# Performance work log

Measured on AMD Instinct MI355X. Metric: run time of the kernel, lower is better.

Reference implementation:

```python
import jax, jax.numpy as jnp
import numpy as np

N = 500_000          # minibatch nodes
NUM_NODES = 1_000_000  # embedding table rows
F0 = 500_000         # raw feature table rows for ntype 0
DIN = 256            # raw feature dim for ntype 0
D = 128              # embed_size


def setup_inputs() -> dict:
    key = jax.random.key(0)
    k0, k1, k2, k3, k4, k5 = jax.random.split(key, 6)
    feat0 = jax.random.normal(k0, (F0, DIN), dtype=jnp.float32)
    # xavier-uniform-ish scale for the projection
    lim = float(np.sqrt(6.0 / (DIN + D)))
    W0 = jax.random.uniform(k1, (DIN, D), dtype=jnp.float32, minval=-lim, maxval=lim)
    # node_embeds initialized uniform(-1, 1)
    emb_table = jax.random.uniform(k2, (NUM_NODES, D), dtype=jnp.float32, minval=-1.0, maxval=1.0)
    node_ids = jax.random.randint(k3, (N,), 0, NUM_NODES, dtype=jnp.int32)
    node_tids = jax.random.randint(k4, (N,), 0, 2, dtype=jnp.int32)
    type_ids = jax.random.randint(k5, (N,), 0, F0, dtype=jnp.int32)
    return {"feat0": feat0, "W0": W0, "emb_table": emb_table,
            "node_ids": node_ids, "node_tids": node_tids, "type_ids": type_ids}


def reference(feat0, W0, emb_table, node_ids, node_tids, type_ids):
    # Original loops over node types, building per-type blocks and an index
    # map idx so that the final embeds[idx] restores the original node order.
    # That is equivalent to, per node i:
    #   out[i] = feat0[type_ids[i]] @ W0   if node_tids[i] == 0 (featured type)
    #   out[i] = emb_table[node_ids[i]]    if node_tids[i] == 1 (featureless)
    proj = feat0[type_ids] @ W0          # [N, D] gather + tall-skinny matmul
    emb = emb_table[node_ids]            # [N, D] embedding lookup
    is_featured = (node_tids == 0)[:, None]
    return jnp.where(is_featured, proj, emb)
```

## Files before the change

### kernel.cpp

```cpp
#include <hip/hip_runtime.h>
#include <hip/hip_bf16.h>

#define DIN 256
#define DOUT 128
#define NB 64

using short8  = __attribute__((ext_vector_type(8))) short;
using floatx4 = __attribute__((ext_vector_type(4))) float;

__device__ __forceinline__ unsigned short f2bf(float f) {
    union { float f; unsigned u; } x; x.f = f;
    unsigned u = x.u;
    unsigned r = u + 0x7fffu + ((u >> 16) & 1u);
    return (unsigned short)(r >> 16);
}

__global__ void w0_pack_kernel(const float* __restrict__ W0,
                               unsigned short* __restrict__ Bfrag) {
    int e = blockIdx.x * blockDim.x + threadIdx.x;
    int j  = e & 7;
    int l  = (e >> 3) & 63;
    int ks = (e >> 9) & 7;
    int wt = e >> 12;
    int k = ks * 32 + (l >> 4) * 8 + j;
    int c = wt * 16 + (l & 15);
    Bfrag[e] = f2bf(W0[k * DOUT + c]);
}

__global__ __launch_bounds__(512) void fused_embed_kernel(
    const float* __restrict__ feat0,
    const float* __restrict__ emb_table,
    const unsigned short* __restrict__ Bfrag,
    const int* __restrict__ node_ids,
    const int* __restrict__ node_tids,
    const int* __restrict__ type_ids,
    float* __restrict__ out,
    int n)
{
    __shared__ unsigned short sA[NB * DIN];
    __shared__ unsigned char  sFeat[NB];

    const int t    = threadIdx.x;
    const int base = blockIdx.x * NB;
    const int w    = t >> 6;
    const int l    = t & 63;

    short8 bf[8];
    {
        const short8* bsrc = reinterpret_cast<const short8*>(Bfrag);
        #pragma unroll
        for (int ks = 0; ks < 8; ++ks)
            bf[ks] = bsrc[(w * 8 + ks) * 64 + l];
    }

    {
        const int m = t >> 3;
        const int p = t & 7;
        const int i = base + m;
        int tid = 1;
        if (i < n) tid = node_tids[i];
        const bool featured = (i < n) && (tid == 0);
        if (p == 0) sFeat[m] = featured ? 1 : 0;

        if (featured) {
            const float* src = feat0 + (long long)type_ids[i] * DIN;
            float4 v[8];
            #pragma unroll
            for (int j = 0; j < 8; ++j)
                v[j] = *reinterpret_cast<const float4*>(src + j * 32 + p * 4);
            #pragma unroll
            for (int j = 0; j < 8; ++j) {
                const int k = j * 32 + p * 4;
                ushort4 pk;
                pk.x = f2bf(v[j].x); pk.y = f2bf(v[j].y);
                pk.z = f2bf(v[j].z); pk.w = f2bf(v[j].w);
                const unsigned addr =
                    (unsigned)(m * 512 + k * 2) ^ ((unsigned)(m & 7) << 4);
                *reinterpret_cast<ushort4*>(reinterpret_cast<char*>(sA) + addr) = pk;
            }
        } else if (i < n) {
            const float4* src = reinterpret_cast<const float4*>(
                emb_table + (long long)node_ids[i] * DOUT);
            float4* dst = reinterpret_cast<float4*>(out + (long long)i * DOUT);
            float4 v[4];
            #pragma unroll
            for (int j = 0; j < 4; ++j) v[j] = src[p + j * 8];
            #pragma unroll
            for (int j = 0; j < 4; ++j) dst[p + j * 8] = v[j];
        }
    }
    __syncthreads();

    const int lr = l & 15;
    const int kg = l >> 4;

    floatx4 acc[4];
    #pragma unroll
    for (int rt = 0; rt < 4; ++rt) acc[rt] = (floatx4){0.f, 0.f, 0.f, 0.f};

    #pragma unroll
    for (int ks = 0; ks < 8; ++ks) {
        #pragma unroll
        for (int rt = 0; rt < 4; ++rt) {
            const int row = rt * 16 + lr;
            const unsigned aaddr =
                (unsigned)(row * 512 + ks * 64 + kg * 16) ^ ((unsigned)(row & 7) << 4);
            const short8 af = *reinterpret_cast<const short8*>(
                reinterpret_cast<const char*>(sA) + aaddr);
            acc[rt] = __builtin_amdgcn_mfma_f32_16x16x32_bf16(af, bf[ks], acc[rt], 0, 0, 0);
        }
    }

    const int col = w * 16 + lr;
    #pragma unroll
    for (int rt = 0; rt < 4; ++rt) {
        #pragma unroll
        for (int r = 0; r < 4; ++r) {
            const int row = rt * 16 + kg * 4 + r;
            if (sFeat[row])
                out[(long long)(base + row) * DOUT + col] = acc[rt][r];
        }
    }
}

extern "C" void kernel_launch(void* const* d_in, const int* in_sizes, int n_in,
                              void* d_out, int out_size, void* d_ws, size_t ws_size,
                              hipStream_t stream) {
    const float* feat0      = (const float*)d_in[0];
    const float* W0         = (const float*)d_in[1];
    const float* emb_table  = (const float*)d_in[2];
    const int*   node_ids   = (const int*)d_in[3];
    const int*   node_tids  = (const int*)d_in[4];
    const int*   type_ids   = (const int*)d_in[5];
    float*       out        = (float*)d_out;
    const int n = in_sizes[3];

    unsigned short* Bfrag = (unsigned short*)d_ws;

    hipLaunchKernelGGL(w0_pack_kernel, dim3((DIN * DOUT) / 256), dim3(256),
                       0, stream, W0, Bfrag);

    const int grid = (n + NB - 1) / NB;
    hipLaunchKernelGGL(fused_embed_kernel, dim3(grid), dim3(512), 0, stream,
                       feat0, emb_table, Bfrag, node_ids, node_tids, type_ids, out, n);
}
```

Before: 158.9 us.

## Persistent blocks with double-buffered LDS to overlap gathers with MFMA compute

New measurement: 206.5 us. 1.3x slower.

```diff
diff --git a/kernel.cpp b/kernel.cpp
--- a/kernel.cpp
+++ b/kernel.cpp
@@ -27,7 +27,7 @@
     Bfrag[e] = f2bf(W0[k * DOUT + c]);
 }
 
-__global__ __launch_bounds__(512) void fused_embed_kernel(
+__global__ __launch_bounds__(512, 4) void fused_embed_kernel(
     const float* __restrict__ feat0,
     const float* __restrict__ emb_table,
     const unsigned short* __restrict__ Bfrag,
@@ -35,15 +35,22 @@
     const int* __restrict__ node_tids,
     const int* __restrict__ type_ids,
     float* __restrict__ out,
-    int n)
+    int n, int ntiles, int tpb)
 {
-    __shared__ unsigned short sA[NB * DIN];
-    __shared__ unsigned char  sFeat[NB];
+    __shared__ unsigned short sA[2][NB * DIN];
+    __shared__ unsigned char  sFeat[2][NB];
 
-    const int t    = threadIdx.x;
-    const int base = blockIdx.x * NB;
-    const int w    = t >> 6;
-    const int l    = t & 63;
+    const int t  = threadIdx.x;
+    const int w  = t >> 6;
+    const int l  = t & 63;
+    const int m  = t >> 3;
+    const int p  = t & 7;
+    const int lr = l & 15;
+    const int kg = l >> 4;
+
+    const int t0 = blockIdx.x * tpb;
+    const int t1 = (t0 + tpb < ntiles) ? (t0 + tpb) : ntiles;
+    if (t0 >= t1) return;
 
     short8 bf[8];
     {
@@ -53,21 +60,31 @@
             bf[ks] = bsrc[(w * 8 + ks) * 64 + l];
     }
 
-    {
-        const int m = t >> 3;
-        const int p = t & 7;
-        const int i = base + m;
-        int tid = 1;
-        if (i < n) tid = node_tids[i];
-        const bool featured = (i < n) && (tid == 0);
-        if (p == 0) sFeat[m] = featured ? 1 : 0;
+    int tidA = -1, gtA = 0, gnA = 0;
+    int tidB = -1, gtB = 0, gnB = 0;
+    float4 v[8];
 
-        if (featured) {
-            const float* src = feat0 + (long long)type_ids[i] * DIN;
-            float4 v[8];
+    auto loadIdx = [&](int tt, int& tid, int& gt, int& gn) {
+        const int i = tt * NB + m;
+        if (i < n) { tid = node_tids[i]; gt = type_ids[i]; gn = node_ids[i]; }
+        else tid = -1;
+    };
+    auto issueGather = [&](int tid, int gt, int gn) {
+        if (tid == 0) {
+            const float* src = feat0 + (long long)gt * DIN;
             #pragma unroll
             for (int j = 0; j < 8; ++j)
                 v[j] = *reinterpret_cast<const float4*>(src + j * 32 + p * 4);
+        } else if (tid == 1) {
+            const float4* src = reinterpret_cast<const float4*>(
+                emb_table + (long long)gn * DOUT);
+            #pragma unroll
+            for (int j = 0; j < 4; ++j) v[j] = src[p + j * 8];
+        }
+    };
+    auto commit = [&](int buf, int tt, int tid) {
+        if (tid == 0) {
+            char* basep = reinterpret_cast<char*>(&sA[buf][0]);
             #pragma unroll
             for (int j = 0; j < 8; ++j) {
                 const int k = j * 32 + p * 4;
@@ -76,50 +93,81 @@
                 pk.z = f2bf(v[j].z); pk.w = f2bf(v[j].w);
                 const unsigned addr =
                     (unsigned)(m * 512 + k * 2) ^ ((unsigned)(m & 7) << 4);
-                *reinterpret_cast<ushort4*>(reinterpret_cast<char*>(sA) + addr) = pk;
+                *reinterpret_cast<ushort4*>(basep + addr) = pk;
             }
-        } else if (i < n) {
-            const float4* src = reinterpret_cast<const float4*>(
-                emb_table + (long long)node_ids[i] * DOUT);
+        } else if (tid == 1) {
+            const int i = tt * NB + m;
             float4* dst = reinterpret_cast<float4*>(out + (long long)i * DOUT);
-            float4 v[4];
-            #pragma unroll
-            for (int j = 0; j < 4; ++j) v[j] = src[p + j * 8];
             #pragma unroll
             for (int j = 0; j < 4; ++j) dst[p + j * 8] = v[j];
         }
-    }
+    };
+
+    loadIdx(t0, tidA, gtA, gnA);
+    if (t0 + 1 < t1) loadIdx(t0 + 1, tidB, gtB, gnB);
+    issueGather(tidA, gtA, gnA);
+    if (p == 0) sFeat[0][m] = (tidA == 0) ? 1 : 0;
+    commit(0, t0, tidA);
+    tidA = tidB; gtA = gtB; gnA = gnB;
     __syncthreads();
 
-    const int lr = l & 15;
-    const int kg = l >> 4;
+    for (int tt = t0; tt < t1; ++tt) {
+        const int cur = (tt - t0) & 1;
+        const int nxt = cur ^ 1;
+        const bool hasNext = (tt + 1 < t1);
 
-    floatx4 acc[4];
-    #pragma unroll
-    for (int rt = 0; rt < 4; ++rt) acc[rt] = (floatx4){0.f, 0.f, 0.f, 0.f};
+        if (hasNext) {
+            issueGather(tidA, gtA, gnA);
+            if (p == 0) sFeat[nxt][m] = (tidA == 0) ? 1 : 0;
+        }
+        if (tt + 2 < t1) loadIdx(tt + 2, tidB, gtB, gnB); else tidB = -1;
 
-    #pragma unroll
-    for (int ks = 0; ks < 8; ++ks) {
+        floatx4 acc[4];
+        #pragma unroll
+        for (int rt = 0; rt < 4; ++rt) acc[rt] = (floatx4){0.f, 0.f, 0.f, 0.f};
+        const char* basep = reinterpret_cast<const char*>(&sA[cur][0]);
+        #pragma unroll
+        for (int ks = 0; ks < 8; ++ks) {
+            #pragma unroll
+            for (int rt = 0; rt < 4; ++rt) {
+                const int row = rt * 16 + lr;
+                const unsigned aaddr =
+                    (unsigned)(row * 512 + ks * 64 + kg * 16) ^ ((unsigned)(row & 7) << 4);
+                const short8 af = *reinterpret_cast<const short8*>(basep + aaddr);
+                acc[rt] = __builtin_amdgcn_mfma_f32_16x16x32_bf16(af, bf[ks], acc[rt], 0, 0, 0);
+            }
+        }
+
+        if (hasNext) commit(nxt, tt + 1, tidA);
+
+        bool ok[4];
+        #pragma unroll
+        for (int r = 0; r < 4; ++r) ok[r] = sFeat[cur][kg * 4 + r] != 0
+                                            || false;
+        #pragma unroll
+        for (int r = 0; r < 4; ++r) ok[r] = false;
+        unsigned char okb[16];
+        #pragma unroll
+        for (int rt = 0; rt < 4; ++rt)
+            #pragma unroll
+            for (int r = 0; r < 4; ++r)
+                okb[rt * 4 + r] = sFeat[cur][rt * 16 + kg * 4 + r];
+
+        __syncthreads();
+
+        const int col  = w * 16 + lr;
+        const int base = tt * NB;
         #pragma unroll
         for (int rt = 0; rt < 4; ++rt) {
-            const int row = rt * 16 + lr;
-            const unsigned aaddr =
-                (unsigned)(row * 512 + ks * 64 + kg * 16) ^ ((unsigned)(row & 7) << 4);
-            const short8 af = *reinterpret_cast<const short8*>(
-                reinterpret_cast<const char*>(sA) + aaddr);
-            acc[rt] = __builtin_amdgcn_mfma_f32_16x16x32_bf16(af, bf[ks], acc[rt], 0, 0, 0);
+            #pragma unroll
+            for (int r = 0; r < 4; ++r) {
+                const int row = rt * 16 + kg * 4 + r;
+                if (okb[rt * 4 + r])
+                    out[(long long)(base + row) * DOUT + col] = acc[rt][r];
+            }
         }
-    }
 
-    const int col = w * 16 + lr;
-    #pragma unroll
-    for (int rt = 0; rt < 4; ++rt) {
-        #pragma unroll
-        for (int r = 0; r < 4; ++r) {
-            const int row = rt * 16 + kg * 4 + r;
-            if (sFeat[row])
-                out[(long long)(base + row) * DOUT + col] = acc[rt][r];
-        }
+        tidA = tidB; gtA = gtB; gnA = gnB;
     }
 }
 
@@ -140,7 +188,10 @@
     hipLaunchKernelGGL(w0_pack_kernel, dim3((DIN * DOUT) / 256), dim3(256),
                        0, stream, W0, Bfrag);
 
-    const int grid = (n + NB - 1) / NB;
+    const int ntiles = (n + NB - 1) / NB;
+    const int grid   = 512;
+    const int tpb    = (ntiles + grid - 1) / grid;
     hipLaunchKernelGGL(fused_embed_kernel, dim3(grid), dim3(512), 0, stream,
-                       feat0, emb_table, Bfrag, node_ids, node_tids, type_ids, out, n);
+                       feat0, emb_table, Bfrag, node_ids, node_tids, type_ids,
+                       out, n, ntiles, tpb);
 }
```

## Stage W0 in LDS and stream feat0 rows directly into MFMA registers

Applied to the files above, without the earlier changes.

New measurement: 182.2 us. 14.7% more time.

```diff
diff --git a/kernel.cpp b/kernel.cpp
--- a/kernel.cpp
+++ b/kernel.cpp
@@ -3,7 +3,6 @@
 
 #define DIN 256
 #define DOUT 128
-#define NB 64
 
 using short8  = __attribute__((ext_vector_type(8))) short;
 using floatx4 = __attribute__((ext_vector_type(4))) float;
@@ -21,13 +20,13 @@
     int j  = e & 7;
     int l  = (e >> 3) & 63;
     int ks = (e >> 9) & 7;
-    int wt = e >> 12;
+    int ct = e >> 12;
     int k = ks * 32 + (l >> 4) * 8 + j;
-    int c = wt * 16 + (l & 15);
+    int c = ct * 16 + (l & 15);
     Bfrag[e] = f2bf(W0[k * DOUT + c]);
 }
 
-__global__ __launch_bounds__(512) void fused_embed_kernel(
+__global__ __launch_bounds__(512, 4) void fused_embed_kernel(
     const float* __restrict__ feat0,
     const float* __restrict__ emb_table,
     const unsigned short* __restrict__ Bfrag,
@@ -37,88 +36,77 @@
     float* __restrict__ out,
     int n)
 {
-    __shared__ unsigned short sA[NB * DIN];
-    __shared__ unsigned char  sFeat[NB];
+    __shared__ short8 sB[4096];
 
-    const int t    = threadIdx.x;
-    const int base = blockIdx.x * NB;
-    const int w    = t >> 6;
-    const int l    = t & 63;
+    const int t = threadIdx.x;
+    const int w = t >> 6;
+    const int l = t & 63;
+    const int lr = l & 15;
+    const int kg = l >> 4;
 
-    short8 bf[8];
     {
-        const short8* bsrc = reinterpret_cast<const short8*>(Bfrag);
+        const short8* src = reinterpret_cast<const short8*>(Bfrag);
         #pragma unroll
-        for (int ks = 0; ks < 8; ++ks)
-            bf[ks] = bsrc[(w * 8 + ks) * 64 + l];
+        for (int j = 0; j < 8; ++j) sB[t + j * 512] = src[t + j * 512];
+    }
+
+    const long long nodebase = (long long)blockIdx.x * 128 + w * 16;
+    const long long myrow = nodebase + lr;
+    int tid = 1, gt = 0, gn = 0;
+    if (myrow < n) {
+        tid = node_tids[myrow];
+        gt  = type_ids[myrow];
+        gn  = node_ids[myrow];
+    }
+
+    __syncthreads();
+
+    floatx4 acc[8];
+    #pragma unroll
+    for (int ct = 0; ct < 8; ++ct) acc[ct] = (floatx4){0.f, 0.f, 0.f, 0.f};
+
+    const float4* arow = reinterpret_cast<const float4*>(
+        feat0 + (long long)gt * DIN) + kg * 2;
+    #pragma unroll
+    for (int ks = 0; ks < 8; ++ks) {
+        const float4 a0 = arow[ks * 8];
+        const float4 a1 = arow[ks * 8 + 1];
+        short8 af;
+        af[0] = (short)f2bf(a0.x); af[1] = (short)f2bf(a0.y);
+        af[2] = (short)f2bf(a0.z); af[3] = (short)f2bf(a0.w);
+        af[4] = (short)f2bf(a1.x); af[5] = (short)f2bf(a1.y);
+        af[6] = (short)f2bf(a1.z); af[7] = (short)f2bf(a1.w);
+        #pragma unroll
+        for (int ct = 0; ct < 8; ++ct)
+            acc[ct] = __builtin_amdgcn_mfma_f32_16x16x32_bf16(
+                af, sB[(ct * 8 + ks) * 64 + l], acc[ct], 0, 0, 0);
+    }
+
+    #pragma unroll
+    for (int r = 0; r < 4; ++r) {
+        const int row   = kg * 4 + r;
+        const int t_r   = __shfl(tid, row);
+        const long long node = nodebase + row;
+        if (t_r == 0 && node < n) {
+            float* orow = out + node * DOUT;
+            #pragma unroll
+            for (int ct = 0; ct < 8; ++ct)
+                orow[ct * 16 + lr] = acc[ct][r];
+        }
     }
 
     {
-        const int m = t >> 3;
-        const int p = t & 7;
-        const int i = base + m;
-        int tid = 1;
-        if (i < n) tid = node_tids[i];
-        const bool featured = (i < n) && (tid == 0);
-        if (p == 0) sFeat[m] = featured ? 1 : 0;
-
-        if (featured) {
-            const float* src = feat0 + (long long)type_ids[i] * DIN;
-            float4 v[8];
+        const int crow = l >> 2;
+        const int csub = l & 3;
+        const int t_c  = __shfl(tid, crow);
+        const int gn_c = __shfl(gn, crow);
+        const long long cnode = nodebase + crow;
+        if (t_c == 1 && cnode < n) {
+            const float4* src = reinterpret_cast<const float4*>(
+                emb_table + (long long)gn_c * DOUT);
+            float4* dst = reinterpret_cast<float4*>(out + cnode * DOUT);
             #pragma unroll
-            for (int j = 0; j < 8; ++j)
-                v[j] = *reinterpret_cast<const float4*>(src + j * 32 + p * 4);
-            #pragma unroll
-            for (int j = 0; j < 8; ++j) {
-                const int k = j * 32 + p * 4;
-                ushort4 pk;
-                pk.x = f2bf(v[j].x); pk.y = f2bf(v[j].y);
-                pk.z = f2bf(v[j].z); pk.w = f2bf(v[j].w);
-                const unsigned addr =
-                    (unsigned)(m * 512 + k * 2) ^ ((unsigned)(m & 7) << 4);
-                *reinterpret_cast<ushort4*>(reinterpret_cast<char*>(sA) + addr) = pk;
-            }
-        } else if (i < n) {
-            const float4* src = reinterpret_cast<const float4*>(
-                emb_table + (long long)node_ids[i] * DOUT);
-            float4* dst = reinterpret_cast<float4*>(out + (long long)i * DOUT);
-            float4 v[4];
-            #pragma unroll
-            for (int j = 0; j < 4; ++j) v[j] = src[p + j * 8];
-            #pragma unroll
-            for (int j = 0; j < 4; ++j) dst[p + j * 8] = v[j];
-        }
-    }
-    __syncthreads();
-
-    const int lr = l & 15;
-    const int kg = l >> 4;
-
-    floatx4 acc[4];
-    #pragma unroll
-    for (int rt = 0; rt < 4; ++rt) acc[rt] = (floatx4){0.f, 0.f, 0.f, 0.f};
-
-    #pragma unroll
-    for (int ks = 0; ks < 8; ++ks) {
-        #pragma unroll
-        for (int rt = 0; rt < 4; ++rt) {
-            const int row = rt * 16 + lr;
-            const unsigned aaddr =
-                (unsigned)(row * 512 + ks * 64 + kg * 16) ^ ((unsigned)(row & 7) << 4);
-            const short8 af = *reinterpret_cast<const short8*>(
-                reinterpret_cast<const char*>(sA) + aaddr);
-            acc[rt] = __builtin_amdgcn_mfma_f32_16x16x32_bf16(af, bf[ks], acc[rt], 0, 0, 0);
-        }
-    }
-
-    const int col = w * 16 + lr;
-    #pragma unroll
-    for (int rt = 0; rt < 4; ++rt) {
-        #pragma unroll
-        for (int r = 0; r < 4; ++r) {
-            const int row = rt * 16 + kg * 4 + r;
-            if (sFeat[row])
-                out[(long long)(base + row) * DOUT + col] = acc[rt][r];
+            for (int j = 0; j < 8; ++j) dst[csub + j * 4] = src[csub + j * 4];
         }
     }
 }
@@ -140,7 +128,8 @@
     hipLaunchKernelGGL(w0_pack_kernel, dim3((DIN * DOUT) / 256), dim3(256),
                        0, stream, W0, Bfrag);
 
-    const int grid = (n + NB - 1) / NB;
+    const int grid = (n + 127) / 128;
     hipLaunchKernelGGL(fused_embed_kernel, dim3(grid), dim3(512), 0, stream,
-                       feat0, emb_table, Bfrag, node_ids, node_tids, type_ids, out, n);
+                       feat0, emb_table, Bfrag, node_ids, node_tids, type_ids,
+                       out, n);
 }
```
